# Kernel tuning notes

Hardware: AMD Instinct MI355X
Metric: run time of the kernel (lower is better)

The kernel has to match this reference:

```python
import jax, jax.numpy as jnp
import numpy as np

N, E, S, TS = 12, 7, 1024, 3          # num_boxes, edge_types, state_dim, time_step
D_IN = 1056 * 1 * 5 * 5               # emb_features * continuous_frames * crop_size^2


def _gru(x, h0, Wih, Whh, bih, bhh):
    """PyTorch-order GRU (gates r,z,n) over leading time axis. x: [T, B, S]."""
    def step(h, xt):
        gi = xt @ Wih.T + bih
        gh = h @ Whh.T + bhh
        ir, iz, inn = jnp.split(gi, 3, axis=-1)
        hr, hz, hn = jnp.split(gh, 3, axis=-1)
        r = jax.nn.sigmoid(ir + hr)
        z = jax.nn.sigmoid(iz + hz)
        n = jnp.tanh(inn + r * hn)
        h_new = (1.0 - z) * n + z * h
        return h_new, h_new
    _, ys = jax.lax.scan(step, h0, x)
    return ys


def _forward(pose_features, Wc, bc, We, be, Wcomp, bcomp, Wr, br, Wz, bz, Wh, bh,
             Wih, Whh, bih, bhh, Wa, ba):
    B, T = pose_features.shape[:2]
    BT, BNN = B * T, B * N * N
    # compress_fc: [BT, N, D_IN] -> [BT, N, S]
    prop = pose_features.reshape(BT, N, D_IN) @ Wc.T + bc
    # torch code xavier-normal-inits the GRU h0 each call; we use deterministic keys.
    h0_std = (2.0 / (BNN * S + S)) ** 0.5
    base = jax.random.key(42)
    gs = None
    for t in range(TS + 1):
        # all edge_fcs at once: [BT, N, E, S]
        msgs = jnp.einsum('bnd,esd->bnes', prop, We) + be
        msg_flat = msgs.reshape(BT, N * E, S)       # index n*E+e, matches torch cat+view
        scs = []
        for e in range(E):
            rf = msgs[:, :, e, :]                   # [BT, N, S]
            pair = jnp.concatenate([
                jnp.broadcast_to(rf[:, :, None, :], (BT, N, N, S)),
                jnp.broadcast_to(rf[:, None, :, :], (BT, N, N, S))], axis=-1)
            # -> [T, B*N*N, 2S] (permute(1,0,2,3,4) in torch)
            pair = pair.reshape(B, T, N, N, 2 * S).transpose(1, 0, 2, 3, 4).reshape(T, BNN, 2 * S)
            x = pair @ Wcomp.T + bcomp              # compress: [T, BNN, S]
            h0 = jax.random.normal(jax.random.fold_in(base, t * E + e), (BNN, S), dtype=x.dtype) * h0_std
            y = _gru(x, h0, Wih, Whh, bih, bhh)     # [T, BNN, S]
            y = y.reshape(T, B, N, N, S).transpose(1, 0, 2, 3, 4).reshape(BT, N, N, S)
            # edge attention (Dropout is identity in eval): sigmoid(linear->1)
            scs.append(jax.nn.sigmoid(jnp.einsum('bmns,s->bmn', y, Wa[e]) + ba[e]))
        gs = jnp.stack(scs, axis=-1)                # [BT, N, N, E]
        merged = jnp.einsum('bnm,bms->bns', gs.reshape(BT, N, N * E), msg_flat)
        a = jnp.concatenate([merged, prop], axis=-1)
        r = jax.nn.sigmoid(a @ Wr.T + br)
        z = jax.nn.sigmoid(a @ Wz.T + bz)
        h_hat = jnp.tanh(jnp.concatenate([merged, r * prop], axis=-1) @ Wh.T + bh)
        prop = (1.0 - z) * prop + z * h_hat
    box_states = gs                                 # last graph_scores
    action_score = ((1.0 - box_states[..., :1]) * box_states).sum(axis=2).reshape(B, T, N, E)
    actor_score = (1.0 - box_states[..., 0]).reshape(B, T, N, N)
    acty_score = jax.nn.softmax(
        (action_score * actor_score.sum(axis=-1)[..., None]).sum(axis=2)[:, :, 1:], axis=-1)
    return action_score, acty_score, actor_score


def setup_inputs() -> dict:
    key = jax.random.key(0)
    ks = jax.random.split(key, 16)
    B, T = 2, 4
    k = 1.0 / np.sqrt(S)  # torch GRU default uniform init bound
    return {
        'pose_features': jax.random.normal(ks[0], (B, T, N, D_IN), jnp.float32),
        'boxes_in': jax.random.uniform(ks[1], (B, T, N, 4), jnp.float32),
        'boxes_dhdw': jax.random.normal(ks[2], (B, T, N, 2), jnp.float32),
        'bboxes_num_in': jax.random.randint(ks[3], (B, T), 1, N),
        'actor_label': jax.random.randint(ks[4], (B, T, N), 0, E),
        'Wc': 0.01 * jax.random.normal(ks[5], (S, D_IN), jnp.float32),
        'bc': jnp.zeros((S,), jnp.float32),
        'We': 0.01 * jax.random.normal(ks[6], (E, S, S), jnp.float32),
        'be': jnp.zeros((E, S), jnp.float32),
        'Wcomp': 0.01 * jax.random.normal(ks[7], (S, 2 * S), jnp.float32),
        'bcomp': jnp.zeros((S,), jnp.float32),
        'Wr': 0.01 * jax.random.normal(ks[8], (S, 2 * S), jnp.float32),
        'br': jnp.zeros((S,), jnp.float32),
        'Wz': 0.01 * jax.random.normal(ks[9], (S, 2 * S), jnp.float32),
        'bz': jnp.zeros((S,), jnp.float32),
        'Wh': 0.01 * jax.random.normal(ks[10], (S, 2 * S), jnp.float32),
        'bh': jnp.zeros((S,), jnp.float32),
        'Wih': jax.random.uniform(ks[11], (3 * S, S), jnp.float32, -k, k),
        'Whh': jax.random.uniform(ks[12], (3 * S, S), jnp.float32, -k, k),
        'bih': jax.random.uniform(ks[13], (3 * S,), jnp.float32, -k, k),
        'bhh': jax.random.uniform(ks[14], (3 * S,), jnp.float32, -k, k),
        'Wa': 0.01 * jax.random.normal(ks[15], (E, S), jnp.float32),
        'ba': jnp.zeros((E,), jnp.float32),
    }


def reference(pose_features, boxes_in, boxes_dhdw, bboxes_num_in, actor_label,
              Wc, bc, We, be, Wcomp, bcomp, Wr, br, Wz, bz, Wh, bh,
              Wih, Whh, bih, bhh, Wa, ba):
    # boxes_in / boxes_dhdw / bboxes_num_in / actor_label only provide shapes in eval mode
    del boxes_in, boxes_dhdw, bboxes_num_in, actor_label
    return _forward(pose_features, Wc, bc, We, be, Wcomp, bcomp, Wr, br, Wz, bz,
                    Wh, bh, Wih, Whh, bih, bhh, Wa, ba)
```

## Files before the change

kernel.cpp:

```cpp
#include <hip/hip_runtime.h>
#include <math.h>

#define NQ 12
#define EQ 7
#define SQ 1024
#define TSQ 3
#define DIN 26400
#define BQ 2
#define TQ 4
#define BT 8
#define BNN 288
#define NROWS 2016
#define G3S 3072
#define BK 32

typedef unsigned short u16;
typedef float f32x4 __attribute__((ext_vector_type(4)));
typedef short s16x8 __attribute__((ext_vector_type(8)));

__device__ __forceinline__ short bh(float f) {
    unsigned u = __float_as_uint(f);
    return (short)((u + 0x8000u) >> 16);
}
__device__ __forceinline__ float b2f(u16 u) {
    return __uint_as_float((unsigned)u << 16);
}
__device__ __forceinline__ s16x8 pack8(float4 a, float4 b) {
    s16x8 r;
    r[0] = bh(a.x); r[1] = bh(a.y); r[2] = bh(a.z); r[3] = bh(a.w);
    r[4] = bh(b.x); r[5] = bh(b.y); r[6] = bh(b.z); r[7] = bh(b.w);
    return r;
}
__device__ __forceinline__ void gload16(const void* g, void* l) {
    __builtin_amdgcn_global_load_lds(
        (const __attribute__((address_space(1))) unsigned*)g,
        (__attribute__((address_space(3))) unsigned*)l, 16, 0, 0);
}
__device__ inline float sigmoidf(float x) { return 1.f / (1.f + expf(-x)); }

template<int AS32, int BS32>
__global__ __launch_bounds__(256)
void gemm_mfma(const void* __restrict__ Ap, long sAb, int lda,
               const void* __restrict__ Bp, long sBb, int ldb,
               const float* __restrict__ bias, long sBiasb,
               float* __restrict__ C, long sCb, int ldc,
               u16* __restrict__ Cb, long sCbb, int ldcb,
               int M, int Nn, int K, int act, int ksplit)
{
    __shared__ __align__(16) u16 lA[2][256][8];
    __shared__ __align__(16) u16 lB[2][512][8];

    const int z = blockIdx.z;
    const int az = z / ksplit;
    const int ks = z - az * ksplit;
    const int Ksl = K / ksplit;
    const int kbase = ks * Ksl;

    const char* Abase = (const char*)Ap + (long)az * sAb * (AS32 ? 4 : 2);
    const char* Bbase = (const char*)Bp + (long)az * sBb * (BS32 ? 4 : 2);

    const int tid = threadIdx.x;
    const int lane = tid & 63;
    const int wave = tid >> 6;
    const int row0 = blockIdx.x * 64;
    const int col0 = blockIdx.y * 128;
    const int wcol = wave * 32;

    const int akg = tid >> 6;
    long arow = row0 + (tid & 63); if (arow >= M) arow = M - 1;
    const int bkg0 = tid >> 7;
    const int s1 = tid + 256;
    const int bkg1 = s1 >> 7;
    long brow0 = col0 + (tid & 127); if (brow0 >= Nn) brow0 = Nn - 1;
    long brow1 = col0 + (s1 & 127);  if (brow1 >= Nn) brow1 = Nn - 1;

    const int arw32 = tid >> 2, akg32 = tid & 3;
    long ar32 = row0 + arw32; if (ar32 >= M) ar32 = M - 1;
    const int brw32 = tid >> 1, bh32 = tid & 1;
    long br32 = col0 + brw32; if (br32 >= Nn) br32 = Nn - 1;

    f32x4 acc[4][2] = {};

#define STAGE(b, kt) do {                                                     \
    const int k0_ = kbase + (kt) * BK;                                        \
    if constexpr (AS32) {                                                     \
        const float* A32 = (const float*)Abase;                               \
        const float* p0 = A32 + ar32 * lda + k0_ + akg32 * 8;                 \
        *(s16x8*)&lA[b][akg32 * 64 + arw32][0] =                              \
            pack8(*(const float4*)p0, *(const float4*)(p0 + 4));              \
    } else {                                                                  \
        const u16* A16 = (const u16*)Abase;                                   \
        gload16(A16 + arow * lda + k0_ + akg * 8, &lA[b][tid][0]);            \
    }                                                                         \
    if constexpr (BS32) {                                                     \
        const float* B32 = (const float*)Bbase;                               \
        const float* q0 = B32 + br32 * ldb + k0_ + bh32 * 16;                 \
        *(s16x8*)&lB[b][(bh32 * 2) * 128 + brw32][0] =                        \
            pack8(*(const float4*)q0, *(const float4*)(q0 + 4));              \
        *(s16x8*)&lB[b][(bh32 * 2 + 1) * 128 + brw32][0] =                    \
            pack8(*(const float4*)(q0 + 8), *(const float4*)(q0 + 12));       \
    } else {                                                                  \
        const u16* B16 = (const u16*)Bbase;                                   \
        gload16(B16 + brow0 * ldb + k0_ + bkg0 * 8, &lB[b][tid][0]);          \
        gload16(B16 + brow1 * ldb + k0_ + bkg1 * 8, &lB[b][s1][0]);           \
    }                                                                         \
} while (0)

#define MFMA_BODY(bufi)                                                       \
    {                                                                         \
        s16x8 af[4], bfr[2];                                                  \
        _Pragma("unroll")                                                     \
        for (int m = 0; m < 4; ++m)                                           \
            af[m] = *(const s16x8*)&lA[bufi][kg * 64 + m * 16 + lr][0];       \
        _Pragma("unroll")                                                     \
        for (int n = 0; n < 2; ++n)                                           \
            bfr[n] = *(const s16x8*)&lB[bufi][kg * 128 + wcol + n * 16 + lr][0]; \
        _Pragma("unroll")                                                     \
        for (int m = 0; m < 4; ++m)                                           \
            _Pragma("unroll")                                                 \
            for (int n = 0; n < 2; ++n)                                       \
                acc[m][n] = __builtin_amdgcn_mfma_f32_16x16x32_bf16(af[m], bfr[n], acc[m][n], 0, 0, 0); \
    }

    const int nk = Ksl / BK;
    const int kg = lane >> 4;
    const int lr = lane & 15;
    int buf = 0;

    STAGE(0, 0);
    if constexpr (!AS32 && !BS32) {
        for (int kt = 0; kt < nk; ++kt) {
            if (kt + 1 < nk) {
                STAGE(buf ^ 1, kt + 1);
                asm volatile("s_waitcnt vmcnt(3)" ::: "memory");
            } else {
                asm volatile("s_waitcnt vmcnt(0)" ::: "memory");
            }
            __builtin_amdgcn_s_barrier();
            __builtin_amdgcn_sched_barrier(0);
            MFMA_BODY(buf);
            __builtin_amdgcn_s_barrier();
            buf ^= 1;
        }
    } else {
        __syncthreads();
        for (int kt = 0; kt < nk; ++kt) {
            if (kt + 1 < nk) STAGE(buf ^ 1, kt + 1);
            MFMA_BODY(buf);
            __syncthreads();
            buf ^= 1;
        }
    }
#undef STAGE
#undef MFMA_BODY

    const int ccol = lane & 15;
    const int crow = (lane >> 4) * 4;
#pragma unroll
    for (int n = 0; n < 2; ++n) {
        const int c = col0 + wcol + n * 16 + ccol;
        const float bv = bias ? bias[(long)az * sBiasb + c] : 0.f;
#pragma unroll
        for (int m = 0; m < 4; ++m) {
            const int rb = row0 + m * 16 + crow;
#pragma unroll
            for (int q = 0; q < 4; ++q) {
                const int r = rb + q;
                if (r >= M) continue;
                float v = acc[m][n][q] + bv;
                if (act == 1) v = 1.f / (1.f + expf(-v));
                else if (act == 2) v = tanhf(v);
                if (C)  C[(long)z * sCb + (long)r * ldc + c] = v;
                if (Cb) Cb[(long)z * sCbb + (long)r * ldcb + c] = (u16)bh(v);
            }
        }
    }
}

__global__ __launch_bounds__(256)
void gemm128_f32(const float* __restrict__ A, int lda,
                 const float* __restrict__ Bm, int ldb,
                 float* __restrict__ C, long sCb, int ldc,
                 u16* __restrict__ Cb, int ldcb,
                 int M, int Nn, int K, int ksplit)
{
    __shared__ __align__(16) u16 lA[2][512][8];
    __shared__ __align__(16) u16 lB[2][512][8];

    const int ks = blockIdx.z;
    const int Ksl = K / ksplit;
    const int kbase = ks * Ksl;

    const int tid = threadIdx.x;
    const int lane = tid & 63;
    const int wave = tid >> 6;
    const int row0 = blockIdx.x * 128;
    const int col0 = blockIdx.y * 128;
    const int wrow = (wave >> 1) * 64;
    const int wcol = (wave & 1) * 64;

    const int rw = tid >> 1, hf = tid & 1;
    long ar = row0 + rw; if (ar >= M) ar = M - 1;
    long br = col0 + rw; if (br >= Nn) br = Nn - 1;

    f32x4 acc[4][4] = {};

#define STAGE128(b, kt) do {                                                  \
    const int k0_ = kbase + (kt) * BK;                                        \
    const float* p = A + ar * lda + k0_ + hf * 16;                            \
    *(s16x8*)&lA[b][(hf * 2) * 128 + rw][0] =                                 \
        pack8(*(const float4*)p, *(const float4*)(p + 4));                    \
    *(s16x8*)&lA[b][(hf * 2 + 1) * 128 + rw][0] =                             \
        pack8(*(const float4*)(p + 8), *(const float4*)(p + 12));             \
    const float* q = Bm + br * ldb + k0_ + hf * 16;                           \
    *(s16x8*)&lB[b][(hf * 2) * 128 + rw][0] =                                 \
        pack8(*(const float4*)q, *(const float4*)(q + 4));                    \
    *(s16x8*)&lB[b][(hf * 2 + 1) * 128 + rw][0] =                             \
        pack8(*(const float4*)(q + 8), *(const float4*)(q + 12));             \
} while (0)

    const int nk = Ksl / BK;
    STAGE128(0, 0);
    __syncthreads();
    int buf = 0;
    const int kg = lane >> 4;
    const int lr = lane & 15;
    for (int kt = 0; kt < nk; ++kt) {
        if (kt + 1 < nk) STAGE128(buf ^ 1, kt + 1);
        s16x8 af[4], bfr[4];
#pragma unroll
        for (int m = 0; m < 4; ++m)
            af[m] = *(const s16x8*)&lA[buf][kg * 128 + wrow + m * 16 + lr][0];
#pragma unroll
        for (int n = 0; n < 4; ++n)
            bfr[n] = *(const s16x8*)&lB[buf][kg * 128 + wcol + n * 16 + lr][0];
#pragma unroll
        for (int m = 0; m < 4; ++m)
#pragma unroll
            for (int n = 0; n < 4; ++n)
                acc[m][n] = __builtin_amdgcn_mfma_f32_16x16x32_bf16(af[m], bfr[n], acc[m][n], 0, 0, 0);
        __syncthreads();
        buf ^= 1;
    }
#undef STAGE128

    const int ccol = lane & 15;
    const int crow = (lane >> 4) * 4;
#pragma unroll
    for (int n = 0; n < 4; ++n) {
        const int c = col0 + wcol + n * 16 + ccol;
#pragma unroll
        for (int m = 0; m < 4; ++m) {
            const int rb = row0 + wrow + m * 16 + crow;
#pragma unroll
            for (int q = 0; q < 4; ++q) {
                const int r = rb + q;
                if (r >= M) continue;
                float v = acc[m][n][q];
                if (C)  C[(long)ks * sCb + (long)r * ldc + c] = v;
                if (Cb) Cb[(long)r * ldcb + c] = (u16)bh(v);
            }
        }
    }
}

__global__ __launch_bounds__(512)
void gh_gru(const u16* __restrict__ hb_in, const u16* __restrict__ Whh_b,
            const float* __restrict__ bhh, const u16* __restrict__ Gnm_b,
            const float* __restrict__ cbias,
            u16* __restrict__ hb_out,
            const float* __restrict__ Wa, float* __restrict__ gs_part, int tt)
{
    __shared__ __align__(16) u16 lA[2][1024][8];
    __shared__ __align__(16) u16 lB[2][1536][8];
    __shared__ float rowdot[128];

    const int f = blockIdx.x;
    const int ly = 2 * (f & 7) + ((f >> 3) & 1);
    const int lx = f >> 4;
    const int row0 = lx * 128;
    const int col0 = ly * 64;

    const int tid = threadIdx.x;
    const int lane = tid & 63;
    const int wave = tid >> 6;
    const int wr = wave >> 1;
    const int wc = wave & 1;

    long arow = row0 + (tid & 127); if (arow >= NROWS) arow = NROWS - 1;

    const u16* aP0 = hb_in + arow * SQ + (tid >> 7) * 8;
    const u16* aP1 = aP0 + 32;
    const u16* bP[3];
#pragma unroll
    for (int j = 0; j < 3; ++j) {
        const int s = tid + j * 512;
        const int bk16 = s / 192;
        const int grow = s - bk16 * 192;
        bP[j] = Whh_b + (long)((grow >> 6) * SQ + col0 + (grow & 63)) * SQ + bk16 * 8;
    }

    f32x4 acc[3][2][2] = {};

#define GSTAGE(b, kt) do {                                                    \
    const int k0_ = (kt) * 64;                                                \
    gload16(aP0 + k0_, &lA[b][tid][0]);                                       \
    gload16(aP1 + k0_, &lA[b][tid + 512][0]);                                 \
    _Pragma("unroll")                                                         \
    for (int j = 0; j < 3; ++j)                                               \
        gload16(bP[j] + k0_, &lB[b][tid + j * 512][0]);                       \
} while (0)

    GSTAGE(0, 0);
    int buf = 0;
    const int kg = lane >> 4;
    const int lr = lane & 15;
    for (int kt = 0; kt < 16; ++kt) {
        if (kt + 1 < 16) {
            GSTAGE(buf ^ 1, kt + 1);
            asm volatile("s_waitcnt vmcnt(5)" ::: "memory");
        } else {
            asm volatile("s_waitcnt vmcnt(0)" ::: "memory");
        }
        __builtin_amdgcn_s_barrier();
        __builtin_amdgcn_sched_barrier(0);
#pragma unroll
        for (int kk = 0; kk < 2; ++kk) {
            const int k16 = kk * 4 + kg;
            s16x8 af[2], bfr[3][2];
#pragma unroll
            for (int m = 0; m < 2; ++m)
                af[m] = *(const s16x8*)&lA[buf][k16 * 128 + wr * 32 + m * 16 + lr][0];
#pragma unroll
            for (int g = 0; g < 3; ++g)
#pragma unroll
                for (int n = 0; n < 2; ++n)
                    bfr[g][n] = *(const s16x8*)&lB[buf][k16 * 192 + g * 64 + wc * 32 + n * 16 + lr][0];
#pragma unroll
            for (int g = 0; g < 3; ++g)
#pragma unroll
                for (int m = 0; m < 2; ++m)
#pragma unroll
                    for (int n = 0; n < 2; ++n)
                        acc[g][m][n] = __builtin_amdgcn_mfma_f32_16x16x32_bf16(af[m], bfr[g][n], acc[g][m][n], 0, 0, 0);
        }
        __builtin_amdgcn_s_barrier();
        buf ^= 1;
    }
#undef GSTAGE

    if (tid < 128) rowdot[tid] = 0.f;
    __syncthreads();

    const int ccol = lane & 15;
    const int crow4 = (lane >> 4) * 4;
    int col2[2];
    float cbv[3][2], bhv[3][2];
#pragma unroll
    for (int n = 0; n < 2; ++n) {
        const int c = col0 + wc * 32 + n * 16 + ccol;
        col2[n] = c;
#pragma unroll
        for (int g = 0; g < 3; ++g) {
            cbv[g][n] = cbias[g * SQ + c];
            bhv[g][n] = bhh[g * SQ + c];
        }
    }

#pragma unroll
    for (int m = 0; m < 2; ++m) {
#pragma unroll
        for (int q = 0; q < 4; ++q) {
            const int row = row0 + wr * 32 + m * 16 + crow4 + q;
            const bool valid = (row < NROWS);
            float d = 0.f;
            if (valid) {
                const int e = row / BNN;
                const int rr = row - e * BNN;
                const int b_ = rr / 144;
                const int ni = (rr / 12) % 12;
                const int mi = rr % 12;
                const int bt = b_ * TQ + tt;
                const u16* gnp = Gnm_b + ((long)e * 96 + bt * 12 + ni) * 6144;
                const u16* gmp = Gnm_b + ((long)e * 96 + bt * 12 + mi) * 6144 + G3S;
                const float* wap = Wa + (long)e * SQ;
#pragma unroll
                for (int n = 0; n < 2; ++n) {
                    const int c = col2[n];
                    float gr  = acc[0][m][n][q] + bhv[0][n] + b2f(gnp[c]) + b2f(gmp[c]) + cbv[0][n];
                    float gz  = acc[1][m][n][q] + bhv[1][n] + b2f(gnp[SQ + c]) + b2f(gmp[SQ + c]) + cbv[1][n];
                    float ghn = acc[2][m][n][q] + bhv[2][n];
                    float gin = b2f(gnp[2 * SQ + c]) + b2f(gmp[2 * SQ + c]) + cbv[2][n];
                    float rg = sigmoidf(gr);
                    float zg = sigmoidf(gz);
                    float nn2 = tanhf(gin + rg * ghn);
                    float hp = b2f(hb_in[(long)row * SQ + c]);
                    float hn = (1.f - zg) * nn2 + zg * hp;
                    hb_out[(long)row * SQ + c] = (u16)bh(hn);
                    d += hn * wap[c];
                }
            }
            d += __shfl_xor(d, 1); d += __shfl_xor(d, 2);
            d += __shfl_xor(d, 4); d += __shfl_xor(d, 8);
            if (valid && ccol == 0)
                atomicAdd(&rowdot[wr * 32 + m * 16 + crow4 + q], d);
        }
    }
    __syncthreads();
    if (tid < 128) {
        const int row = row0 + tid;
        if (row < NROWS) gs_part[((long)tt * 2048 + row) * 16 + ly] = rowdot[tid];
    }
}

__global__ __launch_bounds__(256)
void gru0(const u16* __restrict__ Gnm_b, const float* __restrict__ cbias,
          const float* __restrict__ bhh,
          u16* __restrict__ hb_out,
          const float* __restrict__ Wa, const float* __restrict__ ba,
          float* __restrict__ gs)
{
    const int row = blockIdx.x;
    const int e = row / BNN;
    const int r = row % BNN;
    const int b_ = r / 144;
    const int ni = (r / 12) % 12;
    const int mi = r % 12;
    const int bt = b_ * TQ;

    const u16* gnp = Gnm_b + ((long)e * 96 + bt * 12 + ni) * 6144;
    const u16* gmp = Gnm_b + ((long)e * 96 + bt * 12 + mi) * 6144 + G3S;
    u16* hpb = hb_out + (long)row * SQ;

    const int s = threadIdx.x * 4;

    ushort4 nR = *(const ushort4*)(gnp + s);
    ushort4 nZ = *(const ushort4*)(gnp + SQ + s);
    ushort4 nN = *(const ushort4*)(gnp + 2 * SQ + s);
    ushort4 mR = *(const ushort4*)(gmp + s);
    ushort4 mZ = *(const ushort4*)(gmp + SQ + s);
    ushort4 mN = *(const ushort4*)(gmp + 2 * SQ + s);
    float4 cbR = *(const float4*)(cbias + s);
    float4 cbZ = *(const float4*)(cbias + SQ + s);
    float4 cbN = *(const float4*)(cbias + 2 * SQ + s);
    float4 bhR = *(const float4*)(bhh + s);
    float4 bhZ = *(const float4*)(bhh + SQ + s);
    float4 bhN = *(const float4*)(bhh + 2 * SQ + s);
    float4 wv  = *(const float4*)(Wa + (long)e * SQ + s);

    float4 hn4;
    float dot = 0.f;

#define GRU0_COMP(c, u)                                                       \
    {                                                                         \
        float rg = sigmoidf(b2f(nR.u) + b2f(mR.u) + cbR.c + bhR.c);           \
        float zg = sigmoidf(b2f(nZ.u) + b2f(mZ.u) + cbZ.c + bhZ.c);           \
        float nn = tanhf(b2f(nN.u) + b2f(mN.u) + cbN.c + rg * bhN.c);         \
        float hn = (1.f - zg) * nn;                                           \
        hn4.c = hn;                                                           \
        dot += hn * wv.c;                                                     \
    }
    GRU0_COMP(x, x) GRU0_COMP(y, y) GRU0_COMP(z, z) GRU0_COMP(w, w)
#undef GRU0_COMP

    ushort4 hb4;
    hb4.x = (u16)bh(hn4.x); hb4.y = (u16)bh(hn4.y);
    hb4.z = (u16)bh(hn4.z); hb4.w = (u16)bh(hn4.w);
    *(ushort4*)(hpb + s) = hb4;

    for (int off = 32; off > 0; off >>= 1) dot += __shfl_down(dot, off);
    __shared__ float red[4];
    if ((threadIdx.x & 63) == 0) red[threadIdx.x >> 6] = dot;
    __syncthreads();
    if (threadIdx.x == 0) {
        float tot = red[0] + red[1] + red[2] + red[3] + ba[e];
        gs[((bt * 12 + ni) * 12 + mi) * EQ + e] = sigmoidf(tot);
    }
}

__global__ void gs_fin_all(const float* __restrict__ gs_part, const float* __restrict__ ba,
                           float* __restrict__ gs)
{
    int idx = blockIdx.x * 256 + threadIdx.x;
    if (idx >= 3 * 2048) return;
    const int tt = 1 + (idx >> 11);
    const int row = idx & 2047;
    if (row >= NROWS) return;
    float s = 0.f;
#pragma unroll
    for (int j = 0; j < 16; ++j) s += gs_part[((long)tt * 2048 + row) * 16 + j];
    const int e = row / BNN;
    const int rr = row - e * BNN;
    const int b_ = rr / 144;
    const int ni = (rr / 12) % 12;
    const int mi = rr % 12;
    const int bt = b_ * TQ + tt;
    gs[((bt * 12 + ni) * 12 + mi) * EQ + e] = sigmoidf(s + ba[e]);
}

__global__ __launch_bounds__(256)
void reduce_k(const float* __restrict__ part, int ksplit, int mn, int Nn,
              const float* __restrict__ bias, long sBiasB, int act,
              float* __restrict__ Cf, long sCfB, int ldcf,
              u16* __restrict__ Cb, long sCbB, int ldcb)
{
    int i4 = blockIdx.x * 256 + threadIdx.x;
    int total4 = mn >> 2;
    if (i4 >= total4) return;
    int b = blockIdx.y;
    const float4* p4 = (const float4*)part;
    float4 s = make_float4(0.f, 0.f, 0.f, 0.f);
    for (int ks = 0; ks < ksplit; ++ks) {
        float4 v = p4[(long)(b * ksplit + ks) * total4 + i4];
        s.x += v.x; s.y += v.y; s.z += v.z; s.w += v.w;
    }
    int i = i4 << 2;
    int r = i / Nn, c = i % Nn;
    if (bias) {
        float4 bv = *(const float4*)(bias + (long)b * sBiasB + c);
        s.x += bv.x; s.y += bv.y; s.z += bv.z; s.w += bv.w;
    }
    if (act == 1) {
        s.x = sigmoidf(s.x); s.y = sigmoidf(s.y); s.z = sigmoidf(s.z); s.w = sigmoidf(s.w);
    } else if (act == 2) {
        s.x = tanhf(s.x); s.y = tanhf(s.y); s.z = tanhf(s.z); s.w = tanhf(s.w);
    }
    if (Cf) *(float4*)(Cf + (long)b * sCfB + (long)r * ldcf + c) = s;
    if (Cb) {
        ushort4 o;
        o.x = (u16)bh(s.x); o.y = (u16)bh(s.y); o.z = (u16)bh(s.z); o.w = (u16)bh(s.w);
        *(ushort4*)(Cb + (long)b * sCbB + (long)r * ldcb + c) = o;
    }
}

__global__ __launch_bounds__(256)
void rz_ahat_k(const float* __restrict__ part, const float* __restrict__ brz,
               const float* __restrict__ prop, u16* __restrict__ amat_b,
               float* __restrict__ zbuf)
{
    int i = blockIdx.x * 256 + threadIdx.x;
    int rrow = i >> 10, c = i & 1023;
    float sr = 0.f, sz = 0.f;
#pragma unroll
    for (int ks = 0; ks < 8; ++ks) {
        const float* p = part + (long)ks * 196608 + (long)rrow * 2048;
        sr += p[c]; sz += p[1024 + c];
    }
    float r = sigmoidf(sr + brz[c]);
    float z = sigmoidf(sz + brz[1024 + c]);
    amat_b[(long)rrow * 2048 + 1024 + c] = (u16)bh(r * prop[i]);
    zbuf[i] = z;
}

__global__ __launch_bounds__(256)
void hhat_prop_k(const float* __restrict__ part, const float* __restrict__ bh_,
                 const float* __restrict__ zbuf,
                 float* __restrict__ prop, u16* __restrict__ prop_b)
{
    int i = blockIdx.x * 256 + threadIdx.x;
    float s = 0.f;
#pragma unroll
    for (int ks = 0; ks < 8; ++ks) s += part[(long)ks * 98304 + i];
    float hhat = tanhf(s + bh_[i & 1023]);
    float z = zbuf[i];
    float v = (1.f - z) * prop[i] + z * hhat;
    prop[i] = v;
    prop_b[i] = (u16)bh(v);
}

__global__ void cvt3_bf16_k(const float* __restrict__ s0, u16* __restrict__ d0, int n0,
                            const float* __restrict__ s1, u16* __restrict__ d1, int n1,
                            const float* __restrict__ s2, u16* __restrict__ d2, int n2)
{
    int i = blockIdx.x * 256 + threadIdx.x;
    const float* s; u16* d; int base;
    if (i < n0) { s = s0; d = d0; base = i; }
    else if (i < n0 + n1) { s = s1; d = d1; base = i - n0; }
    else if (i < n0 + n1 + n2) { s = s2; d = d2; base = i - n0 - n1; }
    else return;
    float4 v = ((const float4*)s)[base];
    ushort4 o;
    o.x = (u16)bh(v.x); o.y = (u16)bh(v.y); o.z = (u16)bh(v.z); o.w = (u16)bh(v.w);
    ((ushort4*)d)[base] = o;
}

__global__ __launch_bounds__(256)
void transpose_wc(const float* __restrict__ Wcomp, float* __restrict__ W1T, float* __restrict__ W2T)
{
    __shared__ float t1[32][33];
    __shared__ float t2[32][33];
    const int tx = threadIdx.x & 31;
    const int ty = threadIdx.x >> 5;
    const int d0 = blockIdx.x * 32;
    const int s0 = blockIdx.y * 32;
#pragma unroll
    for (int k = 0; k < 4; ++k) {
        int d = d0 + ty + k * 8;
        t1[ty + k * 8][tx] = Wcomp[(long)d * 2048 + s0 + tx];
        t2[ty + k * 8][tx] = Wcomp[(long)d * 2048 + 1024 + s0 + tx];
    }
    __syncthreads();
#pragma unroll
    for (int k = 0; k < 4; ++k) {
        int s = s0 + ty + k * 8;
        W1T[(long)s * 1024 + d0 + tx] = t1[tx][ty + k * 8];
        W2T[(long)s * 1024 + d0 + tx] = t2[tx][ty + k * 8];
    }
}

__global__ void pack_rz(const float* __restrict__ Wr, const float* __restrict__ Wz,
                        const float* __restrict__ br, const float* __restrict__ bz,
                        u16* __restrict__ Wrz, float* __restrict__ brz)
{
    int i4 = blockIdx.x * 256 + threadIdx.x;
    if (i4 < 512) {
        int c = i4 * 4;
        float4 b = (c < 1024) ? *(const float4*)(br + c) : *(const float4*)(bz + c - 1024);
        *(float4*)(brz + c) = b;
    }
    if (i4 >= 1048576) return;
    int i = i4 * 4;
    int j = i >> 11;
    int c = i & 2047;
    float4 v = (j < 1024) ? *(const float4*)(Wr + (long)j * 2048 + c)
                          : *(const float4*)(Wz + (long)(j - 1024) * 2048 + c);
    ushort4 o;
    o.x = (u16)bh(v.x); o.y = (u16)bh(v.y); o.z = (u16)bh(v.z); o.w = (u16)bh(v.w);
    *(ushort4*)(Wrz + i) = o;
}

__global__ void cbias_k(const float* __restrict__ Wih, const float* __restrict__ bih,
                        const float* __restrict__ bcomp, float* __restrict__ cbias)
{
    int g = blockIdx.x * blockDim.x + threadIdx.x;
    if (g >= G3S) return;
    const float* w = Wih + (long)g * SQ;
    float s = 0.f;
    for (int k = 0; k < SQ; k += 4) {
        float4 wv = *(const float4*)(w + k);
        float4 bv = *(const float4*)(bcomp + k);
        s += wv.x * bv.x + wv.y * bv.y + wv.z * bv.z + wv.w * bv.w;
    }
    cbias[g] = s + bih[g];
}

__global__ __launch_bounds__(256)
void merged_amat_k(const float* __restrict__ gs, const u16* __restrict__ msgs_b,
                   const float* __restrict__ prop, u16* __restrict__ amat_b)
{
    const int bn = blockIdx.x;
    const int bt = bn / 12;
    __shared__ float g[84];
    if (threadIdx.x < 84) g[threadIdx.x] = gs[bn * 84 + threadIdx.x];
    __syncthreads();
    const int s = threadIdx.x * 4;
    float4 acc = make_float4(0.f, 0.f, 0.f, 0.f);
    for (int j = 0; j < 84; ++j) {
        const ushort4 mv = *(const ushort4*)(msgs_b + ((long)(bt * 84 + j)) * SQ + s);
        float gj = g[j];
        acc.x += gj * b2f(mv.x);
        acc.y += gj * b2f(mv.y);
        acc.z += gj * b2f(mv.z);
        acc.w += gj * b2f(mv.w);
    }
    ushort4 o;
    o.x = (u16)bh(acc.x); o.y = (u16)bh(acc.y); o.z = (u16)bh(acc.z); o.w = (u16)bh(acc.w);
    *(ushort4*)(amat_b + (long)bn * 2048 + s) = o;
    float4 pv = *(const float4*)(prop + (long)bn * SQ + s);
    ushort4 o2;
    o2.x = (u16)bh(pv.x); o2.y = (u16)bh(pv.y); o2.z = (u16)bh(pv.z); o2.w = (u16)bh(pv.w);
    *(ushort4*)(amat_b + (long)bn * 2048 + 1024 + s) = o2;
}

__global__ __launch_bounds__(256)
void outputs_k(const float* __restrict__ gs, float* __restrict__ out)
{
    __shared__ float s_act[672];
    __shared__ float s_asum[96];
    int tid = threadIdx.x;
    for (int idx = tid; idx < 672; idx += 256) {
        int bn = idx / 7, e = idx % 7;
        float sum = 0.f;
        for (int m = 0; m < 12; ++m) {
            float g0 = gs[bn * 84 + m * 7];
            sum += (1.f - g0) * gs[bn * 84 + m * 7 + e];
        }
        s_act[idx] = sum;
        out[idx] = sum;
    }
    for (int idx = tid; idx < 96; idx += 256) {
        float a = 0.f;
        for (int m = 0; m < 12; ++m) a += 1.f - gs[idx * 84 + m * 7];
        s_asum[idx] = a;
    }
    for (int idx = tid; idx < 1152; idx += 256) {
        int bn = idx / 12, m = idx % 12;
        out[720 + idx] = 1.f - gs[bn * 84 + m * 7];
    }
    __syncthreads();
    if (tid < 8) {
        float tmp[6];
        float mx = -1e30f;
        for (int e = 1; e < 7; ++e) {
            float sum = 0.f;
            for (int n = 0; n < 12; ++n) {
                int bn = tid * 12 + n;
                sum += s_act[bn * 7 + e] * s_asum[bn];
            }
            tmp[e - 1] = sum;
            mx = fmaxf(mx, sum);
        }
        float den = 0.f;
        for (int e = 0; e < 6; ++e) { tmp[e] = expf(tmp[e] - mx); den += tmp[e]; }
        for (int e = 0; e < 6; ++e) out[672 + tid * 6 + e] = tmp[e] / den;
    }
}

template<int AS32, int BS32>
static void launch_gemm(const void* A, long sAb, int lda,
                        const void* B, long sBb, int ldb,
                        const float* bias, long sBiasb,
                        float* C, long sCb, int ldc,
                        u16* Cb, long sCbb, int ldcb,
                        int M, int Nn, int K, int act, int batch, int ksplit,
                        hipStream_t stream)
{
    dim3 grid((M + 63) / 64, (Nn + 127) / 128, batch * ksplit);
    gemm_mfma<AS32, BS32><<<grid, dim3(256), 0, stream>>>(
        A, sAb, lda, B, sBb, ldb, bias, sBiasb, C, sCb, ldc, Cb, sCbb, ldcb,
        M, Nn, K, act, ksplit);
}

extern "C" void kernel_launch(void* const* d_in, const int* in_sizes, int n_in,
                              void* d_out, int out_size, void* d_ws, size_t ws_size,
                              hipStream_t stream)
{
    const float* pose  = (const float*)d_in[0];
    const float* Wc    = (const float*)d_in[5];
    const float* bc    = (const float*)d_in[6];
    const float* We    = (const float*)d_in[7];
    const float* be    = (const float*)d_in[8];
    const float* Wcomp = (const float*)d_in[9];
    const float* bcomp = (const float*)d_in[10];
    const float* Wr    = (const float*)d_in[11];
    const float* br    = (const float*)d_in[12];
    const float* Wz    = (const float*)d_in[13];
    const float* bz    = (const float*)d_in[14];
    const float* Wh    = (const float*)d_in[15];
    const float* bh_   = (const float*)d_in[16];
    const float* Wih   = (const float*)d_in[17];
    const float* Whh   = (const float*)d_in[18];
    const float* bih   = (const float*)d_in[19];
    const float* bhh   = (const float*)d_in[20];
    const float* Wa    = (const float*)d_in[21];
    const float* ba    = (const float*)d_in[22];

    float* ws = (float*)d_ws;
    float* prop    = ws;
    float* cbias   = prop + 98304;
    float* scratch = cbias + 3072;
    float* gs      = scratch + 8257536;
    float* zbuf    = gs + 8064;
    float* brz     = zbuf + 98304;
    float* gs_part = brz + 2048;
    float* fend    = gs_part + 131072;
    u16* Whh_b  = (u16*)fend;
    u16* Wnm_b  = Whh_b + 3145728;
    u16* Wrz_b  = Wnm_b + 6291456;
    u16* Gnm_b  = Wrz_b + 4194304;
    u16* msgs_b = Gnm_b + 4128768;
    u16* h_b0   = msgs_b + 688128;
    u16* h_b1   = h_b0 + 2064384;
    u16* prop_b = h_b1 + 2064384;
    u16* amat_b = prop_b + 98304;
    u16* pose_b = amat_b + 196608;
    u16* Wc_b   = pose_b + 2534400;

    float* W1T = scratch;
    float* W2T = scratch + 1048576;

    hipLaunchKernelGGL(cvt3_bf16_k, dim3(31947), dim3(256), 0, stream,
                       Whh, Whh_b, 786432, pose, pose_b, 633600, Wc, Wc_b, 6758400);
    hipLaunchKernelGGL(cbias_k, dim3(12), dim3(256), 0, stream, Wih, bih, bcomp, cbias);
    hipLaunchKernelGGL(transpose_wc, dim3(32, 32), dim3(256), 0, stream, Wcomp, W1T, W2T);
    hipLaunchKernelGGL(pack_rz, dim3(4096), dim3(256), 0, stream, Wr, Wz, br, bz, Wrz_b, brz);
    gemm128_f32<<<dim3(24, 8, 1), dim3(256), 0, stream>>>(
        Wih, SQ, W1T, SQ, nullptr, 0, SQ, Wnm_b, SQ, G3S, SQ, SQ, 1);
    gemm128_f32<<<dim3(24, 8, 1), dim3(256), 0, stream>>>(
        Wih, SQ, W2T, SQ, nullptr, 0, SQ, Wnm_b + (long)G3S * SQ, SQ, G3S, SQ, SQ, 1);
    launch_gemm<0, 0>(pose_b, 0, DIN, Wc_b, 0, DIN, nullptr, 0,
                      scratch, 98304, SQ, nullptr, 0, 0, 96, SQ, DIN, 0, 1, 55, stream);
    hipLaunchKernelGGL(reduce_k, dim3(96, 1), dim3(256), 0, stream,
                       scratch, 55, 98304, SQ, bc, 0L, 0,
                       prop, 0L, SQ, prop_b, 0L, SQ);

    for (int t = 0; t <= TSQ; ++t) {
        launch_gemm<0, 1>(prop_b, 0, SQ, We, (long)SQ * SQ, SQ, nullptr, 0,
                          scratch, 98304, SQ, nullptr, 0, 0, 96, SQ, SQ, 0, EQ, 4, stream);
        hipLaunchKernelGGL(reduce_k, dim3(96, EQ), dim3(256), 0, stream,
                           scratch, 4, 98304, SQ, be, (long)SQ, 0,
                           (float*)nullptr, 0L, 0, msgs_b, (long)SQ, EQ * SQ);
        launch_gemm<0, 0>(msgs_b, SQ, EQ * SQ, Wnm_b, 0, SQ, nullptr, 0,
                          nullptr, 0, 0, Gnm_b, 589824, 6 * SQ, 96, 6 * SQ, SQ, 0, EQ, 1, stream);
        hipLaunchKernelGGL(gru0, dim3(NROWS), dim3(256), 0, stream,
                           Gnm_b, cbias, bhh, h_b0, Wa, ba, gs);
        for (int tt = 1; tt < TQ; ++tt) {
            const u16* hin = (tt & 1) ? h_b0 : h_b1;
            u16* hout = (tt & 1) ? h_b1 : h_b0;
            hipLaunchKernelGGL(gh_gru, dim3(256), dim3(512), 0, stream,
                               hin, Whh_b, bhh, Gnm_b, cbias, hout, Wa, gs_part, tt);
        }
        hipLaunchKernelGGL(gs_fin_all, dim3(24), dim3(256), 0, stream, gs_part, ba, gs);
        if (t < TSQ) {
            hipLaunchKernelGGL(merged_amat_k, dim3(96), dim3(256), 0, stream,
                               gs, msgs_b, prop, amat_b);
            launch_gemm<0, 0>(amat_b, 0, 2 * SQ, Wrz_b, 0, 2 * SQ, nullptr, 0,
                              scratch, 196608, 2 * SQ, nullptr, 0, 0, 96, 2 * SQ, 2 * SQ, 0, 1, 8, stream);
            hipLaunchKernelGGL(rz_ahat_k, dim3(384), dim3(256), 0, stream,
                               scratch, brz, prop, amat_b, zbuf);
            launch_gemm<0, 1>(amat_b, 0, 2 * SQ, Wh, 0, 2 * SQ, nullptr, 0,
                              scratch, 98304, SQ, nullptr, 0, 0, 96, SQ, 2 * SQ, 0, 1, 8, stream);
            hipLaunchKernelGGL(hhat_prop_k, dim3(384), dim3(256), 0, stream,
                               scratch, bh_, zbuf, prop, prop_b);
        }
    }

    hipLaunchKernelGGL(outputs_k, dim3(1), dim3(256), 0, stream, gs, (float*)d_out);
}
```

Before: 1.125 ms.

## Fuse GRU time scan into one cooperative kernel with grid syncs

```diff
diff --git a/kernel.cpp b/kernel.cpp
--- a/kernel.cpp
+++ b/kernel.cpp
@@ -1,5 +1,8 @@
 #include <hip/hip_runtime.h>
+#include <hip/hip_cooperative_groups.h>
 #include <math.h>
+
+namespace cg = cooperative_groups;
 
 #define NQ 12
 #define EQ 7
@@ -265,42 +268,132 @@
 }
 
 __global__ __launch_bounds__(512)
-void gh_gru(const u16* __restrict__ hb_in, const u16* __restrict__ Whh_b,
-            const float* __restrict__ bhh, const u16* __restrict__ Gnm_b,
-            const float* __restrict__ cbias,
-            u16* __restrict__ hb_out,
-            const float* __restrict__ Wa, float* __restrict__ gs_part, int tt)
-{
+void gru_scan(const u16* __restrict__ Whh_b, const float* __restrict__ bhh,
+              const u16* __restrict__ Gnm_b, const float* __restrict__ cbias,
+              u16* __restrict__ hb0, u16* __restrict__ hb1,
+              const float* __restrict__ Wa, const float* __restrict__ ba,
+              float* __restrict__ gs_part, float* __restrict__ gs)
+{
+    cg::grid_group gg = cg::this_grid();
+
     __shared__ __align__(16) u16 lA[2][1024][8];
     __shared__ __align__(16) u16 lB[2][1536][8];
     __shared__ float rowdot[128];
+    __shared__ float red[2][4];
 
     const int f = blockIdx.x;
+    const int tid = threadIdx.x;
+    const int lane = tid & 63;
+    const int wave = tid >> 6;
+
+    {
+        const int half = tid >> 8;
+        const int t2 = tid & 255;
+        const int s = t2 * 4;
+        for (int pass = 0; pass < 4; ++pass) {
+            const int row = pass * 512 + f * 2 + half;
+            const bool valid = (row < NROWS);
+            float dot = 0.f;
+            if (valid) {
+                const int e = row / BNN;
+                const int r = row % BNN;
+                const int b_ = r / 144;
+                const int ni = (r / 12) % 12;
+                const int mi = r % 12;
+                const int bt = b_ * TQ;
+                const u16* gnp = Gnm_b + ((long)e * 96 + bt * 12 + ni) * 6144;
+                const u16* gmp = Gnm_b + ((long)e * 96 + bt * 12 + mi) * 6144 + G3S;
+                ushort4 nR = *(const ushort4*)(gnp + s);
+                ushort4 nZ = *(const ushort4*)(gnp + SQ + s);
+                ushort4 nN = *(const ushort4*)(gnp + 2 * SQ + s);
+                ushort4 mR = *(const ushort4*)(gmp + s);
+                ushort4 mZ = *(const ushort4*)(gmp + SQ + s);
+                ushort4 mN = *(const ushort4*)(gmp + 2 * SQ + s);
+                float4 cbR = *(const float4*)(cbias + s);
+                float4 cbZ = *(const float4*)(cbias + SQ + s);
+                float4 cbN = *(const float4*)(cbias + 2 * SQ + s);
+                float4 bhR = *(const float4*)(bhh + s);
+                float4 bhZ = *(const float4*)(bhh + SQ + s);
+                float4 bhN = *(const float4*)(bhh + 2 * SQ + s);
+                float4 wv  = *(const float4*)(Wa + (long)e * SQ + s);
+                float4 hn4;
+#define GRU0_COMP(c, u)                                                       \
+                {                                                             \
+                    float rg = sigmoidf(b2f(nR.u) + b2f(mR.u) + cbR.c + bhR.c); \
+                    float zg = sigmoidf(b2f(nZ.u) + b2f(mZ.u) + cbZ.c + bhZ.c); \
+                    float nn = tanhf(b2f(nN.u) + b2f(mN.u) + cbN.c + rg * bhN.c); \
+                    float hn = (1.f - zg) * nn;                               \
+                    hn4.c = hn;                                               \
+                    dot += hn * wv.c;                                         \
+                }
+                GRU0_COMP(x, x) GRU0_COMP(y, y) GRU0_COMP(z, z) GRU0_COMP(w, w)
+#undef GRU0_COMP
+                ushort4 hb4;
+                hb4.x = (u16)bh(hn4.x); hb4.y = (u16)bh(hn4.y);
+                hb4.z = (u16)bh(hn4.z); hb4.w = (u16)bh(hn4.w);
+                *(ushort4*)(hb0 + (long)row * SQ + s) = hb4;
+            }
+            for (int off = 32; off > 0; off >>= 1) dot += __shfl_down(dot, off);
+            if (lane == 0) red[half][(tid >> 6) & 3] = dot;
+            __syncthreads();
+            if (valid && t2 == 0) {
+                const int e = row / BNN;
+                const int r = row % BNN;
+                const int b_ = r / 144;
+                const int ni = (r / 12) % 12;
+                const int mi = r % 12;
+                const int bt = b_ * TQ;
+                float tot = red[half][0] + red[half][1] + red[half][2] + red[half][3] + ba[e];
+                gs[((bt * 12 + ni) * 12 + mi) * EQ + e] = sigmoidf(tot);
+            }
+            __syncthreads();
+        }
+    }
+    __threadfence();
+    gg.sync();
+    __threadfence();
+
     const int ly = 2 * (f & 7) + ((f >> 3) & 1);
     const int lx = f >> 4;
     const int row0 = lx * 128;
     const int col0 = ly * 64;
-
-    const int tid = threadIdx.x;
-    const int lane = tid & 63;
-    const int wave = tid >> 6;
     const int wr = wave >> 1;
     const int wc = wave & 1;
+    const int kg = lane >> 4;
+    const int lr = lane & 15;
 
     long arow = row0 + (tid & 127); if (arow >= NROWS) arow = NROWS - 1;
-
-    const u16* aP0 = hb_in + arow * SQ + (tid >> 7) * 8;
-    const u16* aP1 = aP0 + 32;
     const u16* bP[3];
 #pragma unroll
     for (int j = 0; j < 3; ++j) {
-        const int s = tid + j * 512;
-        const int bk16 = s / 192;
-        const int grow = s - bk16 * 192;
+        const int sB = tid + j * 512;
+        const int bk16 = sB / 192;
+        const int grow = sB - bk16 * 192;
         bP[j] = Whh_b + (long)((grow >> 6) * SQ + col0 + (grow & 63)) * SQ + bk16 * 8;
     }
 
-    f32x4 acc[3][2][2] = {};
+    const int ccol = lane & 15;
+    const int crow4 = (lane >> 4) * 4;
+    int col2[2];
+    float cbv[3][2], bhv[3][2];
+#pragma unroll
+    for (int n = 0; n < 2; ++n) {
+        const int c = col0 + wc * 32 + n * 16 + ccol;
+        col2[n] = c;
+#pragma unroll
+        for (int g = 0; g < 3; ++g) {
+            cbv[g][n] = cbias[g * SQ + c];
+            bhv[g][n] = bhh[g * SQ + c];
+        }
+    }
+
+    for (int tt = 1; tt <= 3; ++tt) {
+        const u16* hin = (tt & 1) ? hb0 : hb1;
+        u16* hout = (tt & 1) ? hb1 : hb0;
+        const u16* aP0 = hin + arow * SQ + (tid >> 7) * 8;
+        const u16* aP1 = aP0 + 32;
+
+        f32x4 acc[3][2][2] = {};
 
 #define GSTAGE(b, kt) do {                                                    \
     const int k0_ = (kt) * 64;                                                \
@@ -311,191 +404,114 @@
         gload16(bP[j] + k0_, &lB[b][tid + j * 512][0]);                       \
 } while (0)
 
-    GSTAGE(0, 0);
-    int buf = 0;
-    const int kg = lane >> 4;
-    const int lr = lane & 15;
-    for (int kt = 0; kt < 16; ++kt) {
-        if (kt + 1 < 16) {
-            GSTAGE(buf ^ 1, kt + 1);
-            asm volatile("s_waitcnt vmcnt(5)" ::: "memory");
-        } else {
-            asm volatile("s_waitcnt vmcnt(0)" ::: "memory");
-        }
-        __builtin_amdgcn_s_barrier();
-        __builtin_amdgcn_sched_barrier(0);
-#pragma unroll
-        for (int kk = 0; kk < 2; ++kk) {
-            const int k16 = kk * 4 + kg;
-            s16x8 af[2], bfr[3][2];
-#pragma unroll
-            for (int m = 0; m < 2; ++m)
-                af[m] = *(const s16x8*)&lA[buf][k16 * 128 + wr * 32 + m * 16 + lr][0];
-#pragma unroll
-            for (int g = 0; g < 3; ++g)
-#pragma unroll
-                for (int n = 0; n < 2; ++n)
-                    bfr[g][n] = *(const s16x8*)&lB[buf][k16 * 192 + g * 64 + wc * 32 + n * 16 + lr][0];
-#pragma unroll
-            for (int g = 0; g < 3; ++g)
+        GSTAGE(0, 0);
+        int buf = 0;
+        for (int kt = 0; kt < 16; ++kt) {
+            if (kt + 1 < 16) {
+                GSTAGE(buf ^ 1, kt + 1);
+                asm volatile("s_waitcnt vmcnt(5)" ::: "memory");
+            } else {
+                asm volatile("s_waitcnt vmcnt(0)" ::: "memory");
+            }
+            __builtin_amdgcn_s_barrier();
+            __builtin_amdgcn_sched_barrier(0);
+#pragma unroll
+            for (int kk = 0; kk < 2; ++kk) {
+                const int k16 = kk * 4 + kg;
+                s16x8 af[2], bfr[3][2];
 #pragma unroll
                 for (int m = 0; m < 2; ++m)
+                    af[m] = *(const s16x8*)&lA[buf][k16 * 128 + wr * 32 + m * 16 + lr][0];
+#pragma unroll
+                for (int g = 0; g < 3; ++g)
 #pragma unroll
                     for (int n = 0; n < 2; ++n)
-                        acc[g][m][n] = __builtin_amdgcn_mfma_f32_16x16x32_bf16(af[m], bfr[g][n], acc[g][m][n], 0, 0, 0);
-        }
-        __builtin_amdgcn_s_barrier();
-        buf ^= 1;
-    }
+                        bfr[g][n] = *(const s16x8*)&lB[buf][k16 * 192 + g * 64 + wc * 32 + n * 16 + lr][0];
+#pragma unroll
+                for (int g = 0; g < 3; ++g)
+#pragma unroll
+                    for (int m = 0; m < 2; ++m)
+#pragma unroll
+                        for (int n = 0; n < 2; ++n)
+                            acc[g][m][n] = __builtin_amdgcn_mfma_f32_16x16x32_bf16(af[m], bfr[g][n], acc[g][m][n], 0, 0, 0);
+            }
+            __builtin_amdgcn_s_barrier();
+            buf ^= 1;
+        }
 #undef GSTAGE
 
-    if (tid < 128) rowdot[tid] = 0.f;
-    __syncthreads();
-
-    const int ccol = lane & 15;
-    const int crow4 = (lane >> 4) * 4;
-    int col2[2];
-    float cbv[3][2], bhv[3][2];
-#pragma unroll
-    for (int n = 0; n < 2; ++n) {
-        const int c = col0 + wc * 32 + n * 16 + ccol;
-        col2[n] = c;
-#pragma unroll
-        for (int g = 0; g < 3; ++g) {
-            cbv[g][n] = cbias[g * SQ + c];
-            bhv[g][n] = bhh[g * SQ + c];
-        }
-    }
-
-#pragma unroll
-    for (int m = 0; m < 2; ++m) {
-#pragma unroll
-        for (int q = 0; q < 4; ++q) {
-            const int row = row0 + wr * 32 + m * 16 + crow4 + q;
-            const bool valid = (row < NROWS);
-            float d = 0.f;
-            if (valid) {
+        if (tid < 128) rowdot[tid] = 0.f;
+        __syncthreads();
+
+#pragma unroll
+        for (int m = 0; m < 2; ++m) {
+#pragma unroll
+            for (int q = 0; q < 4; ++q) {
+                const int row = row0 + wr * 32 + m * 16 + crow4 + q;
+                const bool valid = (row < NROWS);
+                float d = 0.f;
+                if (valid) {
+                    const int e = row / BNN;
+                    const int rr = row - e * BNN;
+                    const int b_ = rr / 144;
+                    const int ni = (rr / 12) % 12;
+                    const int mi = rr % 12;
+                    const int bt = b_ * TQ + tt;
+                    const u16* gnp = Gnm_b + ((long)e * 96 + bt * 12 + ni) * 6144;
+                    const u16* gmp = Gnm_b + ((long)e * 96 + bt * 12 + mi) * 6144 + G3S;
+                    const float* wap = Wa + (long)e * SQ;
+#pragma unroll
+                    for (int n = 0; n < 2; ++n) {
+                        const int c = col2[n];
+                        float gr  = acc[0][m][n][q] + bhv[0][n] + b2f(gnp[c]) + b2f(gmp[c]) + cbv[0][n];
+                        float gz  = acc[1][m][n][q] + bhv[1][n] + b2f(gnp[SQ + c]) + b2f(gmp[SQ + c]) + cbv[1][n];
+                        float ghn = acc[2][m][n][q] + bhv[2][n];
+                        float gin = b2f(gnp[2 * SQ + c]) + b2f(gmp[2 * SQ + c]) + cbv[2][n];
+                        float rg = sigmoidf(gr);
+                        float zg = sigmoidf(gz);
+                        float nn2 = tanhf(gin + rg * ghn);
+                        float hp = b2f(hin[(long)row * SQ + c]);
+                        float hn = (1.f - zg) * nn2 + zg * hp;
+                        hout[(long)row * SQ + c] = (u16)bh(hn);
+                        d += hn * wap[c];
+                    }
+                }
+                d += __shfl_xor(d, 1); d += __shfl_xor(d, 2);
+                d += __shfl_xor(d, 4); d += __shfl_xor(d, 8);
+                if (valid && ccol == 0)
+                    atomicAdd(&rowdot[wr * 32 + m * 16 + crow4 + q], d);
+            }
+        }
+        __syncthreads();
+        if (tid < 128) {
+            const int row = row0 + tid;
+            if (row < NROWS) gs_part[((long)tt * 2048 + row) * 16 + ly] = rowdot[tid];
+        }
+        __threadfence();
+        gg.sync();
+        __threadfence();
+    }
+
+    {
+        const int gidx = f * 512 + tid;
+        if (gidx < 3 * 2048) {
+            const int tt = 1 + (gidx >> 11);
+            const int row = gidx & 2047;
+            if (row < NROWS) {
+                float sum = 0.f;
+#pragma unroll
+                for (int j = 0; j < 16; ++j)
+                    sum += gs_part[((long)tt * 2048 + row) * 16 + j];
                 const int e = row / BNN;
                 const int rr = row - e * BNN;
                 const int b_ = rr / 144;
                 const int ni = (rr / 12) % 12;
                 const int mi = rr % 12;
                 const int bt = b_ * TQ + tt;
-                const u16* gnp = Gnm_b + ((long)e * 96 + bt * 12 + ni) * 6144;
-                const u16* gmp = Gnm_b + ((long)e * 96 + bt * 12 + mi) * 6144 + G3S;
-                const float* wap = Wa + (long)e * SQ;
-#pragma unroll
-                for (int n = 0; n < 2; ++n) {
-                    const int c = col2[n];
-                    float gr  = acc[0][m][n][q] + bhv[0][n] + b2f(gnp[c]) + b2f(gmp[c]) + cbv[0][n];
-                    float gz  = acc[1][m][n][q] + bhv[1][n] + b2f(gnp[SQ + c]) + b2f(gmp[SQ + c]) + cbv[1][n];
-                    float ghn = acc[2][m][n][q] + bhv[2][n];
-                    float gin = b2f(gnp[2 * SQ + c]) + b2f(gmp[2 * SQ + c]) + cbv[2][n];
-                    float rg = sigmoidf(gr);
-                    float zg = sigmoidf(gz);
-                    float nn2 = tanhf(gin + rg * ghn);
-                    float hp = b2f(hb_in[(long)row * SQ + c]);
-                    float hn = (1.f - zg) * nn2 + zg * hp;
-                    hb_out[(long)row * SQ + c] = (u16)bh(hn);
-                    d += hn * wap[c];
-                }
-            }
-            d += __shfl_xor(d, 1); d += __shfl_xor(d, 2);
-            d += __shfl_xor(d, 4); d += __shfl_xor(d, 8);
-            if (valid && ccol == 0)
-                atomicAdd(&rowdot[wr * 32 + m * 16 + crow4 + q], d);
-        }
-    }
-    __syncthreads();
-    if (tid < 128) {
-        const int row = row0 + tid;
-        if (row < NROWS) gs_part[((long)tt * 2048 + row) * 16 + ly] = rowdot[tid];
-    }
-}
-
-__global__ __launch_bounds__(256)
-void gru0(const u16* __restrict__ Gnm_b, const float* __restrict__ cbias,
-          const float* __restrict__ bhh,
-          u16* __restrict__ hb_out,
-          const float* __restrict__ Wa, const float* __restrict__ ba,
-          float* __restrict__ gs)
-{
-    const int row = blockIdx.x;
-    const int e = row / BNN;
-    const int r = row % BNN;
-    const int b_ = r / 144;
-    const int ni = (r / 12) % 12;
-    const int mi = r % 12;
-    const int bt = b_ * TQ;
-
-    const u16* gnp = Gnm_b + ((long)e * 96 + bt * 12 + ni) * 6144;
-    const u16* gmp = Gnm_b + ((long)e * 96 + bt * 12 + mi) * 6144 + G3S;
-    u16* hpb = hb_out + (long)row * SQ;
-
-    const int s = threadIdx.x * 4;
-
-    ushort4 nR = *(const ushort4*)(gnp + s);
-    ushort4 nZ = *(const ushort4*)(gnp + SQ + s);
-    ushort4 nN = *(const ushort4*)(gnp + 2 * SQ + s);
-    ushort4 mR = *(const ushort4*)(gmp + s);
-    ushort4 mZ = *(const ushort4*)(gmp + SQ + s);
-    ushort4 mN = *(const ushort4*)(gmp + 2 * SQ + s);
-    float4 cbR = *(const float4*)(cbias + s);
-    float4 cbZ = *(const float4*)(cbias + SQ + s);
-    float4 cbN = *(const float4*)(cbias + 2 * SQ + s);
-    float4 bhR = *(const float4*)(bhh + s);
-    float4 bhZ = *(const float4*)(bhh + SQ + s);
-    float4 bhN = *(const float4*)(bhh + 2 * SQ + s);
-    float4 wv  = *(const float4*)(Wa + (long)e * SQ + s);
-
-    float4 hn4;
-    float dot = 0.f;
-
-#define GRU0_COMP(c, u)                                                       \
-    {                                                                         \
-        float rg = sigmoidf(b2f(nR.u) + b2f(mR.u) + cbR.c + bhR.c);           \
-        float zg = sigmoidf(b2f(nZ.u) + b2f(mZ.u) + cbZ.c + bhZ.c);           \
-        float nn = tanhf(b2f(nN.u) + b2f(mN.u) + cbN.c + rg * bhN.c);         \
-        float hn = (1.f - zg) * nn;                                           \
-        hn4.c = hn;                                                           \
-        dot += hn * wv.c;                                                     \
-    }
-    GRU0_COMP(x, x) GRU0_COMP(y, y) GRU0_COMP(z, z) GRU0_COMP(w, w)
-#undef GRU0_COMP
-
-    ushort4 hb4;
-    hb4.x = (u16)bh(hn4.x); hb4.y = (u16)bh(hn4.y);
-    hb4.z = (u16)bh(hn4.z); hb4.w = (u16)bh(hn4.w);
-    *(ushort4*)(hpb + s) = hb4;
-
-    for (int off = 32; off > 0; off >>= 1) dot += __shfl_down(dot, off);
-    __shared__ float red[4];
-    if ((threadIdx.x & 63) == 0) red[threadIdx.x >> 6] = dot;
-    __syncthreads();
-    if (threadIdx.x == 0) {
-        float tot = red[0] + red[1] + red[2] + red[3] + ba[e];
-        gs[((bt * 12 + ni) * 12 + mi) * EQ + e] = sigmoidf(tot);
-    }
-}
-
-__global__ void gs_fin_all(const float* __restrict__ gs_part, const float* __restrict__ ba,
-                           float* __restrict__ gs)
-{
-    int idx = blockIdx.x * 256 + threadIdx.x;
-    if (idx >= 3 * 2048) return;
-    const int tt = 1 + (idx >> 11);
-    const int row = idx & 2047;
-    if (row >= NROWS) return;
-    float s = 0.f;
-#pragma unroll
-    for (int j = 0; j < 16; ++j) s += gs_part[((long)tt * 2048 + row) * 16 + j];
-    const int e = row / BNN;
-    const int rr = row - e * BNN;
-    const int b_ = rr / 144;
-    const int ni = (rr / 12) % 12;
-    const int mi = rr % 12;
-    const int bt = b_ * TQ + tt;
-    gs[((bt * 12 + ni) * 12 + mi) * EQ + e] = sigmoidf(s + ba[e]);
+                gs[((bt * 12 + ni) * 12 + mi) * EQ + e] = sigmoidf(sum + ba[e]);
+            }
+        }
+    }
 }
 
 __global__ __launch_bounds__(256)
@@ -794,6 +810,15 @@
                        scratch, 55, 98304, SQ, bc, 0L, 0,
                        prop, 0L, SQ, prop_b, 0L, SQ);
 
+    const u16* gsc_Whh = Whh_b;   const float* gsc_bhh = bhh;
+    const u16* gsc_Gnm = Gnm_b;   const float* gsc_cb  = cbias;
+    u16* gsc_h0 = h_b0;           u16* gsc_h1 = h_b1;
+    const float* gsc_Wa = Wa;     const float* gsc_ba = ba;
+    float* gsc_gsp = gs_part;     float* gsc_gs = gs;
+    void* gsc_args[] = { (void*)&gsc_Whh, (void*)&gsc_bhh, (void*)&gsc_Gnm, (void*)&gsc_cb,
+                         (void*)&gsc_h0, (void*)&gsc_h1, (void*)&gsc_Wa, (void*)&gsc_ba,
+                         (void*)&gsc_gsp, (void*)&gsc_gs };
+
     for (int t = 0; t <= TSQ; ++t) {
         launch_gemm<0, 1>(prop_b, 0, SQ, We, (long)SQ * SQ, SQ, nullptr, 0,
                           scratch, 98304, SQ, nullptr, 0, 0, 96, SQ, SQ, 0, EQ, 4, stream);
@@ -802,15 +827,7 @@
                            (float*)nullptr, 0L, 0, msgs_b, (long)SQ, EQ * SQ);
         launch_gemm<0, 0>(msgs_b, SQ, EQ * SQ, Wnm_b, 0, SQ, nullptr, 0,
                           nullptr, 0, 0, Gnm_b, 589824, 6 * SQ, 96, 6 * SQ, SQ, 0, EQ, 1, stream);
-        hipLaunchKernelGGL(gru0, dim3(NROWS), dim3(256), 0, stream,
-                           Gnm_b, cbias, bhh, h_b0, Wa, ba, gs);
-        for (int tt = 1; tt < TQ; ++tt) {
-            const u16* hin = (tt & 1) ? h_b0 : h_b1;
-            u16* hout = (tt & 1) ? h_b1 : h_b0;
-            hipLaunchKernelGGL(gh_gru, dim3(256), dim3(512), 0, stream,
-                               hin, Whh_b, bhh, Gnm_b, cbias, hout, Wa, gs_part, tt);
-        }
-        hipLaunchKernelGGL(gs_fin_all, dim3(24), dim3(256), 0, stream, gs_part, ba, gs);
+        hipLaunchCooperativeKernel(gru_scan, dim3(256), dim3(512), gsc_args, 0u, stream);
         if (t < TSQ) {
             hipLaunchKernelGGL(merged_amat_k, dim3(96), dim3(256), 0, stream,
                                gs, msgs_b, prop, amat_b);
```

Measured after the change: 2.995 ms, median of 2. +166.4%, slower.
